# Optimization experiments

Hardware: AMD Instinct MI355X
Metric: run time of the kernel (lower is better)

## Reference

```python
import jax, jax.numpy as jnp
import numpy as np

# db4 analysis filters (pywt.Wavelet('db4').dec_lo / dec_hi)
_DEC_LO = np.array([-0.010597401784997278, 0.032883011666982945, 0.030841381835986965,
                    -0.18703481171888114, -0.02798376941698385, 0.6308807679295904,
                    0.7148465705525415, 0.23037781330885523], dtype=np.float32)
_DEC_HI = np.array([-0.23037781330885523, 0.7148465705525415, -0.6308807679295904,
                    -0.02798376941698385, 0.18703481171888114, 0.030841381835986965,
                    -0.032883011666982945, -0.010597401784997278], dtype=np.float32)
# pytorch_wavelets stores filters reversed (torch conv = correlation); lax.conv is
# also correlation, so use the same reversed filters. Shape [2, 1, L].
_H = jnp.asarray(np.stack([_DEC_LO[::-1], _DEC_HI[::-1]])[:, None, :])

B, SW, SWS, HW, K, J = 2048, 4, 64, 8, 128, 3
DWT_LEN = 84  # 14 (lo, level 3) + 35 (hi1) + 21 (hi2) + 14 (hi3)


def _dwt_level(x, h):
    """One analysis level, mode='reflect' (pytorch_wavelets afb1d). x: [M, N]."""
    N = x.shape[-1]
    L = h.shape[-1]
    outsize = (N + L - 1) // 2          # pywt.dwt_coeff_len, non-periodization
    p = 2 * (outsize - 1) - N + L
    if p % 2 == 1:                       # odd total pad: one extra zero at the end
        x = jnp.pad(x, ((0, 0), (0, 1)))
    x = jnp.pad(x, ((0, 0), (p // 2, p // 2)), mode='reflect')
    y = jax.lax.conv_general_dilated(x[:, None, :], h, (2,), 'VALID')  # [M, 2, out]
    return y[:, 0, :], y[:, 1, :]


def setup_inputs() -> dict:
    key = jax.random.key(0)
    k1, k2, k3 = jax.random.split(key, 3)
    x = jax.random.normal(k1, (B, 1, SW * SWS, HW, HW), dtype=jnp.float32)
    # one Conv3d(1 -> K, kernel=(DWT_LEN, 8, 8)) per subwindow, kaiming-ish init
    fan_in = DWT_LEN * HW * HW
    conv_weight = jax.random.normal(k2, (SW, K, DWT_LEN, HW, HW), dtype=jnp.float32) / np.sqrt(fan_in)
    conv_bias = jax.random.normal(k3, (SW, K), dtype=jnp.float32) * 0.01
    return {"x": x, "conv_weight": conv_weight, "conv_bias": conv_bias}


def reference(x, conv_weight, conv_bias):
    b = x.shape[0]
    # [B,1,T,8,8] -> [B,SW,8,8,SWS]: DWT runs along the time axis of each subwindow
    xt = x[:, 0].reshape(b, SW, SWS, HW, HW).transpose(0, 1, 3, 4, 2)
    xm = xt.reshape(-1, SWS)  # [B*SW*64, 64]
    lo, highs = xm, []
    for _ in range(J):
        lo, hi = _dwt_level(lo, _H)
        highs.append(hi)
    coeffs = jnp.concatenate([lo] + highs, axis=-1)  # [M, 84], order: lo, hi1, hi2, hi3
    c = coeffs.reshape(b, SW, HW, HW, DWT_LEN).transpose(0, 1, 4, 2, 3)  # [B,SW,84,8,8]
    # per-subwindow Conv3d that fully reduces (t,h,w) -> [B, SW, K]
    feat = jnp.einsum('bsthw,skthw->bsk', c, conv_weight) + conv_bias[None]
    # Dropout3d is identity in eval; LeakyReLU default slope 0.01 (typo in source
    # means leakyrelu_negative_slope is never applied)
    return jax.nn.leaky_relu(feat, 0.01).reshape(b, SW * K)
```

## Files before the change

### kernel.cpp

```cpp
#include <hip/hip_runtime.h>
#include <stdint.h>

typedef unsigned int  u32;
typedef unsigned short u16;
typedef __bf16 bf16x8 __attribute__((ext_vector_type(8)));
typedef float  f32x4  __attribute__((ext_vector_type(4)));

__constant__ float GL[8] = { 0.23037781330885523f,  0.7148465705525415f,
                             0.6308807679295904f,  -0.02798376941698385f,
                            -0.18703481171888114f,  0.030841381835986965f,
                             0.032883011666982945f,-0.010597401784997278f };
__constant__ float GH[8] = {-0.010597401784997278f,-0.032883011666982945f,
                             0.030841381835986965f, 0.18703481171888114f,
                            -0.02798376941698385f, -0.6308807679295904f,
                             0.7148465705525415f,  -0.23037781330885523f };

__device__ inline u16 f32_bf16(float f) {
    u32 u = __float_as_uint(f);
    u += 0x7fffu + ((u >> 16) & 1u);
    return (u16)(u >> 16);
}
__device__ inline u32 pack2_bf16(float a, float b) {
    u32 ua = __float_as_uint(a); ua += 0x7fffu + ((ua >> 16) & 1u);
    u32 ub = __float_as_uint(b); ub += 0x7fffu + ((ub >> 16) & 1u);
    return (ua >> 16) | (ub & 0xffff0000u);
}

__global__ __launch_bounds__(256) void fold_w(const float* __restrict__ cw,
                                              u16* __restrict__ Wp) {
    __shared__ float WdL[84 * 64];
    const int tid = threadIdx.x;

    if (tid < 64) {
        const int j = tid;
        float lo1[35], lo2[21];
#pragma unroll
        for (int i = 0; i < 35; ++i) {
            float sl = 0.f, sh = 0.f;
#pragma unroll
            for (int t = 0; t < 8; ++t) {
                int s = 2 * i + t - 6;
                if (s < 0) s = -s;
                if (s >= 64) s = 126 - s;
                float xv = (s == j) ? 1.0f : 0.0f;
                sl += xv * GL[t]; sh += xv * GH[t];
            }
            lo1[i] = sl;
            WdL[(14 + i) * 64 + j] = sh;
        }
#pragma unroll
        for (int i = 0; i < 21; ++i) {
            float sl = 0.f, sh = 0.f;
#pragma unroll
            for (int t = 0; t < 8; ++t) {
                int s = 2 * i + t - 6;
                if (s < 0) s = -s;
                if (s >= 36) s = 70 - s;
                float xv = (s >= 35) ? 0.0f : lo1[s];
                sl += xv * GL[t]; sh += xv * GH[t];
            }
            lo2[i] = sl;
            WdL[(49 + i) * 64 + j] = sh;
        }
#pragma unroll
        for (int i = 0; i < 14; ++i) {
            float sl = 0.f, sh = 0.f;
#pragma unroll
            for (int t = 0; t < 8; ++t) {
                int s = 2 * i + t - 6;
                if (s < 0) s = -s;
                if (s >= 22) s = 42 - s;
                float xv = (s >= 21) ? 0.0f : lo2[s];
                sl += xv * GL[t]; sh += xv * GH[t];
            }
            WdL[i * 64 + j] = sl;
            WdL[(70 + i) * 64 + j] = sh;
        }
    }
    __syncthreads();

    const int sk = blockIdx.x;
    const int hw = tid & 63;
    const int tg = __builtin_amdgcn_readfirstlane((int)(tid >> 6));
    const int t0 = tg * 16;
    const float* wk = cw + (size_t)sk * (84 * 64);
    float acc[16];
#pragma unroll
    for (int j = 0; j < 16; ++j) acc[j] = 0.f;
#pragma unroll 4
    for (int t = 0; t < 84; ++t) {
        float wv = wk[t * 64 + hw];
        const float* Wr = WdL + t * 64 + t0;
#pragma unroll
        for (int j = 0; j < 16; ++j) acc[j] += wv * Wr[j];
    }
    u16* dst = Wp + (size_t)sk * 4096 + hw;
#pragma unroll
    for (int j = 0; j < 16; ++j) dst[(t0 + j) * 64] = f32_bf16(acc[j]);
}

__global__ __launch_bounds__(256) void gemm_dwt(const float* __restrict__ X,
                                                const u16* __restrict__ Wp,
                                                const float* __restrict__ bias,
                                                float* __restrict__ out) {
    const int nh = blockIdx.x;
    const int mt = blockIdx.y;
    const int s  = blockIdx.z;
    const int tid  = threadIdx.x;
    const int lane = tid & 63;
    const int w    = tid >> 6;
    const int fr   = lane & 15;
    const int fq   = (lane >> 4) & 3;

    __shared__ __align__(16) u16 Xl[16 * 64];
    __shared__ __align__(16) u16 Wl[64 * 64];

    const int wrow = tid >> 2;
    const int wc2  = (tid & 3) * 2;
    const u16* wg = Wp + (size_t)(s * 128 + nh * 64 + wrow) * 4096 + wc2 * 8;
    const int ww0 = wrow * 64 + (((wc2    ) ^ (wrow & 7)) << 3);
    const int ww1 = wrow * 64 + (((wc2 + 1) ^ (wrow & 7)) << 3);

    const bool doX = tid < 128;
    const int xrow = (tid >> 3) & 15;
    const int xch  = tid & 7;
    const float* xg = X + (size_t)(mt * 16 + xrow) * 16384 + s * 4096 + xch * 8;
    const int xw = xrow * 64 + ((xch ^ (xrow & 7)) << 3);

    const int sk7 = fr & 7;
    const int ar  = fr * 64;
    const int br  = (w * 16 + fr) * 64;

    f32x4 acc = {0.f, 0.f, 0.f, 0.f};

    float4 xa, xb; uint4 wa, wb;
    {
        const uint4* wp4 = reinterpret_cast<const uint4*>(wg);
        wa = wp4[0]; wb = wp4[1];
        if (doX) {
            const float4* xp = reinterpret_cast<const float4*>(xg);
            xa = xp[0]; xb = xp[1];
        }
    }

    for (int kt = 0; kt < 64; ++kt) {
        __syncthreads();
        if (doX) {
            uint4 p;
            p.x = pack2_bf16(xa.x, xa.y); p.y = pack2_bf16(xa.z, xa.w);
            p.z = pack2_bf16(xb.x, xb.y); p.w = pack2_bf16(xb.z, xb.w);
            *reinterpret_cast<uint4*>(&Xl[xw]) = p;
        }
        *reinterpret_cast<uint4*>(&Wl[ww0]) = wa;
        *reinterpret_cast<uint4*>(&Wl[ww1]) = wb;
        __syncthreads();
        {
            const int kn = (kt + 1 < 64) ? kt + 1 : 63;
            const uint4* wp4 = reinterpret_cast<const uint4*>(wg + (size_t)kn * 64);
            wa = wp4[0]; wb = wp4[1];
            if (doX) {
                const float4* xp = reinterpret_cast<const float4*>(xg + (size_t)kn * 64);
                xa = xp[0]; xb = xp[1];
            }
        }
#pragma unroll
        for (int h = 0; h < 2; ++h) {
            const int q  = h * 4 + fq;
            const int co = ((q ^ sk7) << 3);
            bf16x8 a = *reinterpret_cast<const bf16x8*>(&Xl[ar + co]);
            bf16x8 b = *reinterpret_cast<const bf16x8*>(&Wl[br + co]);
            acc = __builtin_amdgcn_mfma_f32_16x16x32_bf16(a, b, acc, 0, 0, 0);
        }
    }

    const int colg = s * 128 + nh * 64 + w * 16 + fr;
    const float bv = bias[colg];
    float* og = out + (size_t)(mt * 16) * 512 + colg;
#pragma unroll
    for (int r = 0; r < 4; ++r) {
        const int row = fq * 4 + r;
        float v = acc[r] + bv;
        og[(size_t)row * 512] = v > 0.f ? v : 0.01f * v;
    }
}

extern "C" void kernel_launch(void* const* d_in, const int* in_sizes, int n_in,
                              void* d_out, int out_size, void* d_ws, size_t ws_size,
                              hipStream_t stream) {
    const float* x  = (const float*)d_in[0];
    const float* cw = (const float*)d_in[1];
    const float* cb = (const float*)d_in[2];
    float* out = (float*)d_out;

    u16* Wp = (u16*)d_ws;

    fold_w<<<512, 256, 0, stream>>>(cw, Wp);
    gemm_dwt<<<dim3(2, 128, 4), 256, 0, stream>>>(x, Wp, cb, out);
}
```

Measured before the change: 251.7 us.

## Replace LDS-tiled GEMM with split-K register-direct MFMA GEMM and reduction

The folded weights are rewritten in an MFMA-fragment-ready layout so each wave can load its B operands straight from global memory without LDS staging or block barriers. Each wave computes a 16x128 output tile for one subwindow over a slice of K, so every X row is read once instead of twice. Split-K partial sums are written to workspace and a separate reduce kernel adds them together with the bias and applies LeakyReLU. This adds a third launch and extra partial-sum traffic in exchange for more parallelism and no synchronisation in the main loop.

```diff
diff --git a/kernel.cpp b/kernel.cpp
--- a/kernel.cpp
+++ b/kernel.cpp
@@ -5,6 +5,7 @@
 typedef unsigned short u16;
 typedef __bf16 bf16x8 __attribute__((ext_vector_type(8)));
 typedef float  f32x4  __attribute__((ext_vector_type(4)));
+typedef u32    u32x4  __attribute__((ext_vector_type(4)));
 
 __constant__ float GL[8] = { 0.23037781330885523f,  0.7148465705525415f,
                              0.6308807679295904f,  -0.02798376941698385f,
@@ -27,7 +28,7 @@
 }
 
 __global__ __launch_bounds__(256) void fold_w(const float* __restrict__ cw,
-                                              u16* __restrict__ Wp) {
+                                              u16* __restrict__ Wf) {
     __shared__ float WdL[84 * 64];
     const int tid = threadIdx.x;
 
@@ -80,6 +81,8 @@
     __syncthreads();
 
     const int sk = blockIdx.x;
+    const int s  = sk >> 7;
+    const int n  = sk & 127;
     const int hw = tid & 63;
     const int tg = __builtin_amdgcn_readfirstlane((int)(tid >> 6));
     const int t0 = tg * 16;
@@ -88,100 +91,93 @@
 #pragma unroll
     for (int j = 0; j < 16; ++j) acc[j] = 0.f;
 #pragma unroll 4
-    for (int t = 0; t < 84; ++t) {
-        float wv = wk[t * 64 + hw];
-        const float* Wr = WdL + t * 64 + t0;
+    for (int tau = 0; tau < 84; ++tau) {
+        float wv = wk[tau * 64 + hw];
+        const float* Wr = WdL + tau * 64 + t0;
 #pragma unroll
         for (int j = 0; j < 16; ++j) acc[j] += wv * Wr[j];
     }
-    u16* dst = Wp + (size_t)sk * 4096 + hw;
-#pragma unroll
-    for (int j = 0; j < 16; ++j) dst[(t0 + j) * 64] = f32_bf16(acc[j]);
-}
-
-__global__ __launch_bounds__(256) void gemm_dwt(const float* __restrict__ X,
-                                                const u16* __restrict__ Wp,
-                                                const float* __restrict__ bias,
-                                                float* __restrict__ out) {
-    const int nh = blockIdx.x;
-    const int mt = blockIdx.y;
-    const int s  = blockIdx.z;
+    const int nt = n >> 4;
+    const int fr = n & 15;
+    const int fq = (hw >> 3) & 3;
+    const int jj = hw & 7;
+    const int kbh = hw >> 5;
+#pragma unroll
+    for (int j = 0; j < 16; ++j) {
+        const int t = t0 + j;
+        const size_t idx =
+            ((((size_t)(s * 8 + nt)) * 128 + t * 2 + kbh) * 64 + fq * 16 + fr) * 8 + jj;
+        Wf[idx] = f32_bf16(acc[j]);
+    }
+}
+
+template <int NKB>
+__global__ __launch_bounds__(256, 3) void gemm2(const float* __restrict__ X,
+                                                const u16* __restrict__ Wf,
+                                                float* __restrict__ P) {
     const int tid  = threadIdx.x;
     const int lane = tid & 63;
-    const int w    = tid >> 6;
+    const int gw   = blockIdx.x * 4 + (tid >> 6);
+    const int ksid = gw >> 9;
+    const int rem  = gw & 511;
+    const int s    = rem >> 7;
+    const int mt   = rem & 127;
     const int fr   = lane & 15;
-    const int fq   = (lane >> 4) & 3;
-
-    __shared__ __align__(16) u16 Xl[16 * 64];
-    __shared__ __align__(16) u16 Wl[64 * 64];
-
-    const int wrow = tid >> 2;
-    const int wc2  = (tid & 3) * 2;
-    const u16* wg = Wp + (size_t)(s * 128 + nh * 64 + wrow) * 4096 + wc2 * 8;
-    const int ww0 = wrow * 64 + (((wc2    ) ^ (wrow & 7)) << 3);
-    const int ww1 = wrow * 64 + (((wc2 + 1) ^ (wrow & 7)) << 3);
-
-    const bool doX = tid < 128;
-    const int xrow = (tid >> 3) & 15;
-    const int xch  = tid & 7;
-    const float* xg = X + (size_t)(mt * 16 + xrow) * 16384 + s * 4096 + xch * 8;
-    const int xw = xrow * 64 + ((xch ^ (xrow & 7)) << 3);
-
-    const int sk7 = fr & 7;
-    const int ar  = fr * 64;
-    const int br  = (w * 16 + fr) * 64;
-
-    f32x4 acc = {0.f, 0.f, 0.f, 0.f};
-
-    float4 xa, xb; uint4 wa, wb;
-    {
-        const uint4* wp4 = reinterpret_cast<const uint4*>(wg);
-        wa = wp4[0]; wb = wp4[1];
-        if (doX) {
-            const float4* xp = reinterpret_cast<const float4*>(xg);
-            xa = xp[0]; xb = xp[1];
-        }
-    }
-
-    for (int kt = 0; kt < 64; ++kt) {
-        __syncthreads();
-        if (doX) {
-            uint4 p;
-            p.x = pack2_bf16(xa.x, xa.y); p.y = pack2_bf16(xa.z, xa.w);
-            p.z = pack2_bf16(xb.x, xb.y); p.w = pack2_bf16(xb.z, xb.w);
-            *reinterpret_cast<uint4*>(&Xl[xw]) = p;
-        }
-        *reinterpret_cast<uint4*>(&Wl[ww0]) = wa;
-        *reinterpret_cast<uint4*>(&Wl[ww1]) = wb;
-        __syncthreads();
-        {
-            const int kn = (kt + 1 < 64) ? kt + 1 : 63;
-            const uint4* wp4 = reinterpret_cast<const uint4*>(wg + (size_t)kn * 64);
-            wa = wp4[0]; wb = wp4[1];
-            if (doX) {
-                const float4* xp = reinterpret_cast<const float4*>(xg + (size_t)kn * 64);
-                xa = xp[0]; xb = xp[1];
-            }
-        }
-#pragma unroll
-        for (int h = 0; h < 2; ++h) {
-            const int q  = h * 4 + fq;
-            const int co = ((q ^ sk7) << 3);
-            bf16x8 a = *reinterpret_cast<const bf16x8*>(&Xl[ar + co]);
-            bf16x8 b = *reinterpret_cast<const bf16x8*>(&Wl[br + co]);
-            acc = __builtin_amdgcn_mfma_f32_16x16x32_bf16(a, b, acc, 0, 0, 0);
-        }
-    }
-
-    const int colg = s * 128 + nh * 64 + w * 16 + fr;
-    const float bv = bias[colg];
-    float* og = out + (size_t)(mt * 16) * 512 + colg;
-#pragma unroll
-    for (int r = 0; r < 4; ++r) {
-        const int row = fq * 4 + r;
-        float v = acc[r] + bv;
-        og[(size_t)row * 512] = v > 0.f ? v : 0.01f * v;
-    }
+    const int fq   = lane >> 4;
+    const int kb0  = ksid * NKB;
+
+    const float* xg = X + (size_t)(mt * 16 + fr) * 16384 + s * 4096 + kb0 * 32 + fq * 8;
+    const u16*   wg = Wf + (((size_t)(s * 8) * 128) + kb0) * 512 + lane * 8;
+
+    f32x4 acc[8];
+#pragma unroll
+    for (int nt = 0; nt < 8; ++nt) acc[nt] = (f32x4){0.f, 0.f, 0.f, 0.f};
+
+    f32x4 a0 = __builtin_nontemporal_load(reinterpret_cast<const f32x4*>(xg));
+    f32x4 a1 = __builtin_nontemporal_load(reinterpret_cast<const f32x4*>(xg) + 1);
+
+#pragma unroll 2
+    for (int kb = 0; kb < NKB; ++kb) {
+        union { u32 u[4]; bf16x8 v; } av;
+        av.u[0] = pack2_bf16(a0.x, a0.y); av.u[1] = pack2_bf16(a0.z, a0.w);
+        av.u[2] = pack2_bf16(a1.x, a1.y); av.u[3] = pack2_bf16(a1.z, a1.w);
+        const int kn = (kb + 1 < NKB) ? kb + 1 : kb;
+        a0 = __builtin_nontemporal_load(reinterpret_cast<const f32x4*>(xg + (size_t)kn * 32));
+        a1 = __builtin_nontemporal_load(reinterpret_cast<const f32x4*>(xg + (size_t)kn * 32) + 1);
+        const u16* wb = wg + (size_t)kb * 512;
+#pragma unroll
+        for (int nt = 0; nt < 8; ++nt) {
+            bf16x8 bf = *reinterpret_cast<const bf16x8*>(wb + (size_t)nt * 65536);
+            acc[nt] = __builtin_amdgcn_mfma_f32_16x16x32_bf16(av.v, bf, acc[nt], 0, 0, 0);
+        }
+    }
+
+    float* pg = P + (size_t)ksid * (2048 * 512) + (size_t)(mt * 16) * 512 + s * 128 + fr;
+#pragma unroll
+    for (int nt = 0; nt < 8; ++nt)
+#pragma unroll
+        for (int r = 0; r < 4; ++r)
+            __builtin_nontemporal_store(acc[nt][r], pg + (size_t)(fq * 4 + r) * 512 + nt * 16);
+}
+
+__global__ __launch_bounds__(256) void reduce_k(const float* __restrict__ P,
+                                                const float* __restrict__ bias,
+                                                float* __restrict__ out, int nks) {
+    const int t = blockIdx.x * 256 + threadIdx.x;
+    const size_t base = (size_t)t * 4;
+    f32x4 sum = {0.f, 0.f, 0.f, 0.f};
+    for (int k = 0; k < nks; ++k) {
+        f32x4 v = __builtin_nontemporal_load(
+            reinterpret_cast<const f32x4*>(P + (size_t)k * (2048 * 512) + base));
+        sum += v;
+    }
+    const f32x4 b = *reinterpret_cast<const f32x4*>(bias + (base & 511));
+    f32x4 o = sum + b;
+    o.x = o.x > 0.f ? o.x : 0.01f * o.x;
+    o.y = o.y > 0.f ? o.y : 0.01f * o.y;
+    o.z = o.z > 0.f ? o.z : 0.01f * o.z;
+    o.w = o.w > 0.f ? o.w : 0.01f * o.w;
+    __builtin_nontemporal_store(o, reinterpret_cast<f32x4*>(out + base));
 }
 
 extern "C" void kernel_launch(void* const* d_in, const int* in_sizes, int n_in,
@@ -192,8 +188,20 @@
     const float* cb = (const float*)d_in[2];
     float* out = (float*)d_out;
 
-    u16* Wp = (u16*)d_ws;
-
-    fold_w<<<512, 256, 0, stream>>>(cw, Wp);
-    gemm_dwt<<<dim3(2, 128, 4), 256, 0, stream>>>(x, Wp, cb, out);
-}
+    u16*   Wf = (u16*)d_ws;
+    float* P  = (float*)((char*)d_ws + (4u << 20));
+
+    const size_t MN = (size_t)2048 * 512 * 4;
+    int ks = (ws_size >= (4u << 20) + 8 * MN) ? 8
+           : (ws_size >= (4u << 20) + 4 * MN) ? 4
+           : (ws_size >= (4u << 20) + 2 * MN) ? 2 : 1;
+
+    fold_w<<<512, 256, 0, stream>>>(cw, Wf);
+    switch (ks) {
+        case 8: gemm2<16> <<<128 * 8, 256, 0, stream>>>(x, Wf, P); break;
+        case 4: gemm2<32> <<<128 * 4, 256, 0, stream>>>(x, Wf, P); break;
+        case 2: gemm2<64> <<<128 * 2, 256, 0, stream>>>(x, Wf, P); break;
+        default: gemm2<128><<<128 * 1, 256, 0, stream>>>(x, Wf, P); break;
+    }
+    reduce_k<<<1024, 256, 0, stream>>>(P, cb, out, ks);
+}
```

New measurement: 246.1 us. 2.2% less time.
